# Kernel tuning notes

Measured on AMD Instinct MI355X. Metric: run time of the kernel, lower is better.

The kernel has to match this reference:

```python
import jax, jax.numpy as jnp
import numpy as np

S1 = (42, 1600, 1408); S2 = (21, 800, 704); S3 = (11, 400, 352); S4 = (6, 200, 176)
OFF = np.array([[dz, dy, dx] for dz in (-1, 0, 1) for dy in (-1, 0, 1) for dx in (-1, 0, 1)], np.int64)
KOFF = np.array([[kz, ky, kx] for kz in (0, 1, 2) for ky in (0, 1, 2) for kx in (0, 1, 2)], np.int64)

def _keys(c, s):
    return (c[:, 0] * s[1] + c[:, 1]) * s[2] + c[:, 2]

def _lookup(skeys, qk, valid):
    pos = np.searchsorted(skeys, qk)
    posc = np.clip(pos, 0, len(skeys) - 1)
    found = valid & (skeys[posc] == qk)
    return np.where(found, posc, -1).astype(np.int32)

def _subm_nbr(coords, skeys, shape):
    N = len(coords); nbr = np.empty((N, 27), np.int32); sh = np.array(shape)
    for t in range(27):
        q = coords + OFF[t]
        valid = np.all((q >= 0) & (q < sh), axis=1)
        nbr[:, t] = _lookup(skeys, _keys(q, shape), valid)
    return nbr

def _inv_nbr(fcoords, ckeys, cshape):
    # inverse of stride-2, pad-1, k-3 sparse conv: coarse = (fine + 1 - k) / 2
    N = len(fcoords); nbr = np.empty((N, 27), np.int32); csh = np.array(cshape)
    for t in range(27):
        cand = fcoords + 1 - KOFF[t]
        valid = np.all(cand >= 0, axis=1) & np.all(cand % 2 == 0, axis=1)
        cc = cand // 2
        valid &= np.all(cc < csh, axis=1)
        nbr[:, t] = _lookup(ckeys, _keys(cc, cshape), valid)
    return nbr

def _geometry():
    rng = np.random.default_rng(0)
    n = 130000
    c = np.stack([rng.integers(0, S1[i], n) for i in range(3)], 1).astype(np.int64)
    uk, idx = np.unique(_keys(c, S1), return_index=True)
    c1 = c[idx][:100000]; k1 = uk[:len(c1)]
    def down(cf, s):
        cc = cf // 2
        uk, idx = np.unique(_keys(cc, s), return_index=True)
        return cc[idx], uk
    c2, k2 = down(c1, S2); c3, k3 = down(c2, S3); c4, k4 = down(c3, S4)
    return dict(nbr4=_subm_nbr(c4, k4, S4), inv43=_inv_nbr(c3, k4, S4),
                nbr3=_subm_nbr(c3, k3, S3), inv32=_inv_nbr(c2, k3, S3),
                nbr2=_subm_nbr(c2, k2, S2), inv21=_inv_nbr(c1, k2, S2),
                nbr1=_subm_nbr(c1, k1, S1), n4=len(c4), n1=len(c1))

_SPECS = [("m4", 64, 64), ("i4", 64, 64), ("m3", 64, 64), ("i3", 64, 32),
          ("m2", 32, 32), ("i2", 32, 16), ("m1", 16, 16), ("c5", 16, 3)]

def _params(key):
    p = {}
    for i, (nm, ci, co) in enumerate(_SPECS):
        k = jax.random.fold_in(key, i)
        p["W_" + nm] = jax.random.normal(k, (27, ci, co), jnp.float32) * (1.0 / np.sqrt(27.0 * ci))
        p["g_" + nm] = jnp.ones((co,), jnp.float32)
        p["b_" + nm] = jnp.zeros((co,), jnp.float32)
    return p

def setup_inputs() -> dict:
    geo = _geometry()
    key = jax.random.key(0)
    inp = {k: jnp.asarray(v) for k, v in geo.items() if k.startswith(("nbr", "inv"))}
    inp["x"] = jax.random.normal(jax.random.fold_in(key, 100), (geo["n4"], 64), jnp.float32)
    inp.update(_params(key))
    return inp

def _block(f, nbr, W, g, b, relu=True):
    # gather-GEMM (sparse conv), then BatchNorm1d (training mode, eps=1e-3), then ReLU
    m = nbr >= 0                                             # [N,27]
    x = jnp.where(m[..., None], f[jnp.maximum(nbr, 0)], 0.0)  # [N,27,Cin]
    y = jnp.einsum('nkc,kcd->nd', x, W)                      # [N,Cout]
    mu = y.mean(0); var = y.var(0)
    y = (y - mu) * jax.lax.rsqrt(var + 1e-3) * g + b
    return jax.nn.relu(y) if relu else y

def reference(x, nbr4, inv43, nbr3, inv32, nbr2, inv21, nbr1,
              W_m4, g_m4, b_m4, W_i4, g_i4, b_i4, W_m3, g_m3, b_m3, W_i3, g_i3, b_i3,
              W_m2, g_m2, b_m2, W_i2, g_i2, b_i2, W_m1, g_m1, b_m1, W_c5, g_c5, b_c5):
    h = _block(x, nbr4, W_m4, g_m4, b_m4)      # subm4: [N4,64]
    h = _block(h, inv43, W_i4, g_i4, b_i4)     # inverse conv4 -> [N3,64]
    h = _block(h, nbr3, W_m3, g_m3, b_m3)      # subm3
    h = _block(h, inv32, W_i3, g_i3, b_i3)     # inverse conv3 -> [N2,32]
    h = _block(h, nbr2, W_m2, g_m2, b_m2)      # subm2
    h = _block(h, inv21, W_i2, g_i2, b_i2)     # inverse conv2 -> [N1,16]
    h = _block(h, nbr1, W_m1, g_m1, b_m1)      # subm1
    return _block(h, nbr1, W_c5, g_c5, b_c5, relu=False)  # conv5 (shares subm1 rulebook), BN only
```

## Files before the change

### kernel.cpp

```cpp
#include <hip/hip_runtime.h>

typedef _Float16 HALF;
typedef _Float16 f16x8 __attribute__((ext_vector_type(8)));
typedef float f32x4 __attribute__((ext_vector_type(4)));
typedef int i32x4 __attribute__((ext_vector_type(4)));

struct WArgs { const float* W[8]; HALF* dst[8]; };

__global__ void convert_all_w_kernel(WArgs a)
{
    const int CIs[8]  = {64, 64, 64, 64, 32, 32, 16, 16};
    const int COs[8]  = {64, 64, 64, 32, 32, 16, 16, 3};
    const int COPs[8] = {64, 64, 64, 32, 32, 16, 16, 16};
    const int L = blockIdx.y;
    const int CI = CIs[L], CO = COs[L], COP = COPs[L];
    const int K = 27 * CI, KP = (K + 31) & ~31;
    const int total = COP * KP;
    for (int i = blockIdx.x * 256 + threadIdx.x; i < total; i += gridDim.x * 256) {
        int jp = i / KP;
        int kp = i - jp * KP;
        float v = (jp < CO && kp < K) ? a.W[L][(size_t)kp * CO + jp] : 0.f;
        a.dst[L][((size_t)(kp >> 5) * COP + jp) * 32 + (kp & 31)] = (HALF)v;
    }
}

__global__ void convert_x_kernel(const float* __restrict__ x, HALF* __restrict__ xh, int total)
{
    int i = blockIdx.x * 256 + threadIdx.x;
    if (i < total) xh[i] = (HALF)x[i];
}

template<int CI, int CO_PAD, int NMT, bool FUSED>
__global__ __launch_bounds__(256, 2) void conv_kernel(
    const HALF* __restrict__ h, const int* __restrict__ nbr,
    const HALF* __restrict__ Wt, HALF* __restrict__ yout,
    float* __restrict__ sums, int n,
    const float* __restrict__ psums, const float* __restrict__ pg,
    const float* __restrict__ pb, float pinvn)
{
    constexpr int K    = 27 * CI;
    constexpr int KP   = (K + 31) & ~31;
    constexpr int NCH  = KP / 32;
    constexpr int NJB  = CO_PAD / 16;
    constexpr int NW   = 4;
    constexpr int NCB  = (CI >= 64) ? 2 : 1;
    constexpr int LOG2CI = (CI == 64) ? 6 : ((CI == 32) ? 5 : 4);
    constexpr int NIDX = (CI == 16) ? 14 : 27;

    __shared__ float red[2][NW][CO_PAD];

    const int wv   = threadIdx.x >> 6;
    const int lane = threadIdx.x & 63;
    const int l15  = lane & 15;
    const int lq   = lane >> 4;
    const int waveRow = blockIdx.x * (NW * 16 * NMT) + wv * (16 * NMT);

    f32x4 acc[NMT][NJB];
#pragma unroll
    for (int mt = 0; mt < NMT; ++mt)
#pragma unroll
        for (int jb = 0; jb < NJB; ++jb)
#pragma unroll
            for (int r = 0; r < 4; ++r) acc[mt][jb][r] = 0.f;

    int idxr[NMT][NIDX];
#pragma unroll
    for (int mt = 0; mt < NMT; ++mt) {
        const int row  = waveRow + mt * 16 + l15;
        const bool rok = row < n;
        const int* nb  = nbr + (size_t)min(row, n - 1) * 27;
#pragma unroll
        for (int s = 0; s < NIDX; ++s) {
            const int t = (CI == 16) ? (2 * s + (lq >> 1)) : s;
            const int v = nb[t < 27 ? t : 26];
            idxr[mt][s] = (rok && t < 27) ? v : -1;
        }
    }

    f16x8 sc8[NCB], bi8[NCB];
    if constexpr (FUSED) {
#pragma unroll
        for (int cb = 0; cb < NCB; ++cb) {
            const int c0 = cb * 32 + ((lq * 8) & (CI - 1));
#pragma unroll
            for (int j = 0; j < 8; ++j) {
                const int c = c0 + j;
                const float mu  = psums[c] * pinvn;
                const float var = psums[CI + c] * pinvn - mu * mu;
                const float sc  = rsqrtf(var + 1e-3f) * pg[c];
                sc8[cb][j] = (HALF)sc;
                bi8[cb][j] = (HALF)(pb[c] - mu * sc);
            }
        }
    }

#pragma unroll
    for (int kc = 0; kc < NCH; ++kc) {
        const int c   = (kc * 32 + lq * 8) & (CI - 1);
        const int slot = (CI == 64) ? (kc >> 1) : kc;
        const int ccb  = (NCB == 2) ? (kc & 1) : 0;

        const HALF* wb = Wt + (size_t)kc * (CO_PAD * 32) + lq * 8;
        f16x8 b[NJB];
#pragma unroll
        for (int jb = 0; jb < NJB; ++jb)
            b[jb] = *(const f16x8*)(wb + (size_t)(jb * 16 + l15) * 32);

#pragma unroll
        for (int mt = 0; mt < NMT; ++mt) {
            const int idx = idxr[mt][slot];
            const int off = (max(idx, 0) << LOG2CI) + c;
            f16x8 a = *(const f16x8*)(h + off);
            if constexpr (FUSED) {
                a = a * sc8[ccb] + bi8[ccb];
#pragma unroll
                for (int j = 0; j < 8; ++j)
                    a[j] = (a[j] < (HALF)0.f) ? (HALF)0.f : a[j];
            }
            const int m = ~(idx >> 31);
            i32x4 ai = __builtin_bit_cast(i32x4, a);
            ai.x &= m; ai.y &= m; ai.z &= m; ai.w &= m;
            a = __builtin_bit_cast(f16x8, ai);
#pragma unroll
            for (int jb = 0; jb < NJB; ++jb)
                acc[mt][jb] = __builtin_amdgcn_mfma_f32_16x16x32_f16(a, b[jb], acc[mt][jb], 0, 0, 0);
        }
    }

#pragma unroll
    for (int jb = 0; jb < NJB; ++jb) {
        const int col = jb * 16 + l15;
        float s = 0.f, sq = 0.f;
#pragma unroll
        for (int mt = 0; mt < NMT; ++mt) {
            const int rb = waveRow + mt * 16 + lq * 4;
#pragma unroll
            for (int r = 0; r < 4; ++r) {
                if (rb + r < n) {
                    const float v = acc[mt][jb][r];
                    yout[(size_t)(rb + r) * CO_PAD + col] = (HALF)v;
                    s += v;
                    sq += v * v;
                }
            }
        }
        s  += __shfl_xor(s, 16);  s  += __shfl_xor(s, 32);
        sq += __shfl_xor(sq, 16); sq += __shfl_xor(sq, 32);
        if (lane < 16) { red[0][wv][col] = s; red[1][wv][col] = sq; }
    }
    __syncthreads();
    if (threadIdx.x < CO_PAD) {
        float s = 0.f, sq = 0.f;
#pragma unroll
        for (int w = 0; w < NW; ++w) { s += red[0][w][threadIdx.x]; sq += red[1][w][threadIdx.x]; }
        atomicAdd(&sums[threadIdx.x], s);
        atomicAdd(&sums[CO_PAD + threadIdx.x], sq);
    }
}

__global__ void bn_out_kernel(const HALF* __restrict__ y, const float* __restrict__ sums,
                              const float* __restrict__ g, const float* __restrict__ b,
                              int n, float invn, float* __restrict__ out)
{
    int i = blockIdx.x * 256 + threadIdx.x;
    if (i >= n * 3) return;
    int row = i / 3;
    int c = i - row * 3;
    float mu  = sums[c] * invn;
    float var = sums[16 + c] * invn - mu * mu;
    float sc  = rsqrtf(var + 1e-3f) * g[c];
    out[i] = ((float)y[(size_t)row * 16 + c] - mu) * sc + b[c];
}

extern "C" void kernel_launch(void* const* d_in, const int* in_sizes, int n_in,
                              void* d_out, int out_size, void* d_ws, size_t ws_size,
                              hipStream_t stream)
{
    const int* nbr4  = (const int*)d_in[0];
    const int* inv43 = (const int*)d_in[1];
    const int* nbr3  = (const int*)d_in[2];
    const int* inv32 = (const int*)d_in[3];
    const int* nbr2  = (const int*)d_in[4];
    const int* inv21 = (const int*)d_in[5];
    const int* nbr1  = (const int*)d_in[6];
    const float* x   = (const float*)d_in[7];

    const int n4 = in_sizes[0] / 27;
    const int n3 = in_sizes[1] / 27;
    const int n2 = in_sizes[3] / 27;
    const int n1 = in_sizes[5] / 27;

    const int CIs[8]  = {64, 64, 64, 64, 32, 32, 16, 16};
    const int COPs[8] = {64, 64, 64, 32, 32, 16, 16, 16};
    int KPs[8], wtoff[8];
    int wtot = 0;
    for (int s = 0; s < 8; ++s) {
        KPs[s] = ((27 * CIs[s] + 31) / 32) * 32;
        wtoff[s] = wtot;
        wtot += COPs[s] * KPs[s];
    }

    char* ws = (char*)d_ws;
    HALF* wt = (HALF*)ws;
    size_t off = ((size_t)wtot * sizeof(HALF) + 255) & ~(size_t)255;
    float* sums = (float*)(ws + off);
    off += 8 * 128 * sizeof(float);
    off = (off + 255) & ~(size_t)255;
    HALF* xh = (HALF*)(ws + off);
    off += ((size_t)n4 * 64 * sizeof(HALF) + 255) & ~(size_t)255;
    size_t bufElems = 0;
    {
        size_t cand[4] = {(size_t)n4 * 64, (size_t)n3 * 64, (size_t)n2 * 32, (size_t)n1 * 16};
        for (int i = 0; i < 4; ++i) if (cand[i] > bufElems) bufElems = cand[i];
    }
    HALF* Y0 = (HALF*)(ws + off);
    off += (bufElems * sizeof(HALF) + 255) & ~(size_t)255;
    HALF* Y1 = (HALF*)(ws + off);

    hipMemsetAsync(sums, 0, 8 * 128 * sizeof(float), stream);

    WArgs wa;
    for (int s = 0; s < 8; ++s) { wa.W[s] = (const float*)d_in[8 + 3 * s]; wa.dst[s] = wt + wtoff[s]; }
    {
        int maxTotal = 64 * KPs[0];
        dim3 grid((maxTotal + 255) / 256, 8);
        convert_all_w_kernel<<<grid, 256, 0, stream>>>(wa);
    }
    convert_x_kernel<<<(n4 * 64 + 255) / 256, 256, 0, stream>>>(x, xh, n4 * 64);

#define G(s) ((const float*)d_in[9 + 3 * (s)])
#define B(s) ((const float*)d_in[10 + 3 * (s)])
#define SUMS(s) (sums + (s) * 128)
#define GRID(nn) (((nn) + 127) / 128)

    conv_kernel<64, 64, 2, false><<<GRID(n4), 256, 0, stream>>>(
        xh, nbr4, wt + wtoff[0], Y0, SUMS(0), n4, nullptr, nullptr, nullptr, 0.f);
    conv_kernel<64, 64, 2, true><<<GRID(n3), 256, 0, stream>>>(
        Y0, inv43, wt + wtoff[1], Y1, SUMS(1), n3, SUMS(0), G(0), B(0), 1.f / n4);
    conv_kernel<64, 64, 2, true><<<GRID(n3), 256, 0, stream>>>(
        Y1, nbr3, wt + wtoff[2], Y0, SUMS(2), n3, SUMS(1), G(1), B(1), 1.f / n3);
    conv_kernel<64, 32, 2, true><<<GRID(n2), 256, 0, stream>>>(
        Y0, inv32, wt + wtoff[3], Y1, SUMS(3), n2, SUMS(2), G(2), B(2), 1.f / n3);
    conv_kernel<32, 32, 2, true><<<GRID(n2), 256, 0, stream>>>(
        Y1, nbr2, wt + wtoff[4], Y0, SUMS(4), n2, SUMS(3), G(3), B(3), 1.f / n2);
    conv_kernel<32, 16, 2, true><<<GRID(n1), 256, 0, stream>>>(
        Y0, inv21, wt + wtoff[5], Y1, SUMS(5), n1, SUMS(4), G(4), B(4), 1.f / n2);
    conv_kernel<16, 16, 2, true><<<GRID(n1), 256, 0, stream>>>(
        Y1, nbr1, wt + wtoff[6], Y0, SUMS(6), n1, SUMS(5), G(5), B(5), 1.f / n1);
    conv_kernel<16, 16, 2, true><<<GRID(n1), 256, 0, stream>>>(
        Y0, nbr1, wt + wtoff[7], Y1, SUMS(7), n1, SUMS(6), G(6), B(6), 1.f / n1);
    bn_out_kernel<<<(n1 * 3 + 255) / 256, 256, 0, stream>>>(
        Y1, SUMS(7), G(7), B(7), n1, 1.f / n1, (float*)d_out);

#undef G
#undef B
#undef SUMS
#undef GRID
}
```

Before: 571.6 us.

## Software-pipeline neighbor gathers two chunks ahead and remap blocks across XCDs

Stops preloading all 27 neighbor indices into registers at kernel start. Indices and gathered feature vectors are now fetched two K-chunks ahead in a double-buffered register pipeline, so gather latency overlaps the MFMA work. Block IDs are also remapped so that consecutive row tiles land on the same XCD, which should improve L2 locality. The change lowers register use from the index array but adds dependent index-then-feature loads inside the loop. For CI=64 the same index is loaded twice.

```diff
diff --git a/kernel.cpp b/kernel.cpp
--- a/kernel.cpp
+++ b/kernel.cpp
@@ -45,7 +45,6 @@
     constexpr int NW   = 4;
     constexpr int NCB  = (CI >= 64) ? 2 : 1;
     constexpr int LOG2CI = (CI == 64) ? 6 : ((CI == 32) ? 5 : 4);
-    constexpr int NIDX = (CI == 16) ? 14 : 27;
 
     __shared__ float red[2][NW][CO_PAD];
 
@@ -53,7 +52,15 @@
     const int lane = threadIdx.x & 63;
     const int l15  = lane & 15;
     const int lq   = lane >> 4;
-    const int waveRow = blockIdx.x * (NW * 16 * NMT) + wv * (16 * NMT);
+
+    int bid = blockIdx.x;
+    {
+        const int nwg = gridDim.x;
+        const int q = nwg >> 3, r = nwg & 7;
+        const int xcd = bid & 7, idx = bid >> 3;
+        bid = (xcd < r ? xcd * (q + 1) : r * (q + 1) + (xcd - r) * q) + idx;
+    }
+    const int waveRow = bid * (NW * 16 * NMT) + wv * (16 * NMT);
 
     f32x4 acc[NMT][NJB];
 #pragma unroll
@@ -63,18 +70,13 @@
 #pragma unroll
             for (int r = 0; r < 4; ++r) acc[mt][jb][r] = 0.f;
 
-    int idxr[NMT][NIDX];
+    int  nbo[NMT];
+    bool rok[NMT];
 #pragma unroll
     for (int mt = 0; mt < NMT; ++mt) {
-        const int row  = waveRow + mt * 16 + l15;
-        const bool rok = row < n;
-        const int* nb  = nbr + (size_t)min(row, n - 1) * 27;
-#pragma unroll
-        for (int s = 0; s < NIDX; ++s) {
-            const int t = (CI == 16) ? (2 * s + (lq >> 1)) : s;
-            const int v = nb[t < 27 ? t : 26];
-            idxr[mt][s] = (rok && t < 27) ? v : -1;
-        }
+        const int row = waveRow + mt * 16 + l15;
+        rok[mt] = row < n;
+        nbo[mt] = min(row, n - 1) * 27;
     }
 
     f16x8 sc8[NCB], bi8[NCB];
@@ -94,11 +96,27 @@
         }
     }
 
+    #define TAPOF(kc) ((CI == 16) ? (2 * (kc) + (lq >> 1)) : ((CI == 64) ? ((kc) >> 1) : (kc)))
+    #define CHOF(kc)  (((kc) * 32 + lq * 8) & (CI - 1))
+
+    int   ipf[2][NMT];
+    f16x8 apf[2][NMT];
+#pragma unroll
+    for (int p = 0; p < 2; ++p) {
+#pragma unroll
+        for (int mt = 0; mt < NMT; ++mt) {
+            const int t   = TAPOF(p);
+            const int v   = nbr[nbo[mt] + (t < 27 ? t : 26)];
+            const int idx = (rok[mt] && t < 27) ? v : -1;
+            ipf[p][mt] = idx;
+            apf[p][mt] = *(const f16x8*)(h + ((max(idx, 0) << LOG2CI) + CHOF(p)));
+        }
+    }
+
 #pragma unroll
     for (int kc = 0; kc < NCH; ++kc) {
-        const int c   = (kc * 32 + lq * 8) & (CI - 1);
-        const int slot = (CI == 64) ? (kc >> 1) : kc;
-        const int ccb  = (NCB == 2) ? (kc & 1) : 0;
+        const int cur = kc & 1;
+        const int ccb = (NCB == 2) ? (kc & 1) : 0;
 
         const HALF* wb = Wt + (size_t)kc * (CO_PAD * 32) + lq * 8;
         f16x8 b[NJB];
@@ -106,18 +124,32 @@
         for (int jb = 0; jb < NJB; ++jb)
             b[jb] = *(const f16x8*)(wb + (size_t)(jb * 16 + l15) * 32);
 
+        f16x8 a_use[NMT];
+        int   i_use[NMT];
+#pragma unroll
+        for (int mt = 0; mt < NMT; ++mt) { a_use[mt] = apf[cur][mt]; i_use[mt] = ipf[cur][mt]; }
+
+        if (kc + 2 < NCH) {
+#pragma unroll
+            for (int mt = 0; mt < NMT; ++mt) {
+                const int t   = TAPOF(kc + 2);
+                const int v   = nbr[nbo[mt] + (t < 27 ? t : 26)];
+                const int idx = (rok[mt] && t < 27) ? v : -1;
+                ipf[cur][mt] = idx;
+                apf[cur][mt] = *(const f16x8*)(h + ((max(idx, 0) << LOG2CI) + CHOF(kc + 2)));
+            }
+        }
+
 #pragma unroll
         for (int mt = 0; mt < NMT; ++mt) {
-            const int idx = idxr[mt][slot];
-            const int off = (max(idx, 0) << LOG2CI) + c;
-            f16x8 a = *(const f16x8*)(h + off);
+            f16x8 a = a_use[mt];
             if constexpr (FUSED) {
                 a = a * sc8[ccb] + bi8[ccb];
 #pragma unroll
                 for (int j = 0; j < 8; ++j)
                     a[j] = (a[j] < (HALF)0.f) ? (HALF)0.f : a[j];
             }
-            const int m = ~(idx >> 31);
+            const int m = ~(i_use[mt] >> 31);
             i32x4 ai = __builtin_bit_cast(i32x4, a);
             ai.x &= m; ai.y &= m; ai.z &= m; ai.w &= m;
             a = __builtin_bit_cast(f16x8, ai);
@@ -126,6 +158,8 @@
                 acc[mt][jb] = __builtin_amdgcn_mfma_f32_16x16x32_f16(a, b[jb], acc[mt][jb], 0, 0, 0);
         }
     }
+    #undef TAPOF
+    #undef CHOF
 
 #pragma unroll
     for (int jb = 0; jb < NJB; ++jb) {
```

New measurement: 568.1 us. Within noise of the previous version (-0.6%).

## Software-pipeline gather loads with inline asm, stage rulebook in LDS, remap blocks per XCD

Applied to the files above, without the earlier changes.

Neighbor indices for the block are now staged in shared memory instead of being held in per-thread registers. The A-gather and weight loads are issued through inline-asm global loads three chunks ahead, with explicit vmcnt waits, so memory latency overlaps the MFMA work. Block IDs are also remapped so consecutive rows land on the same XCD, which should improve L2 locality. The cost is fragile manual waitcnt accounting, extra LDS traffic and a syncthreads per block, and more live registers for the prefetch slots.

```diff
diff --git a/kernel.cpp b/kernel.cpp
--- a/kernel.cpp
+++ b/kernel.cpp
@@ -30,6 +30,17 @@
     if (i < total) xh[i] = (HALF)x[i];
 }
 
+#define WAITV(N) do { \
+    if      ((N) == 18) asm volatile("s_waitcnt vmcnt(18)" ::: "memory"); \
+    else if ((N) == 12) asm volatile("s_waitcnt vmcnt(12)" ::: "memory"); \
+    else if ((N) == 9)  asm volatile("s_waitcnt vmcnt(9)"  ::: "memory"); \
+    else if ((N) == 8)  asm volatile("s_waitcnt vmcnt(8)"  ::: "memory"); \
+    else if ((N) == 6)  asm volatile("s_waitcnt vmcnt(6)"  ::: "memory"); \
+    else if ((N) == 4)  asm volatile("s_waitcnt vmcnt(4)"  ::: "memory"); \
+    else if ((N) == 3)  asm volatile("s_waitcnt vmcnt(3)"  ::: "memory"); \
+    else                asm volatile("s_waitcnt vmcnt(0)"  ::: "memory"); \
+} while (0)
+
 template<int CI, int CO_PAD, int NMT, bool FUSED>
 __global__ __launch_bounds__(256, 2) void conv_kernel(
     const HALF* __restrict__ h, const int* __restrict__ nbr,
@@ -45,36 +56,32 @@
     constexpr int NW   = 4;
     constexpr int NCB  = (CI >= 64) ? 2 : 1;
     constexpr int LOG2CI = (CI == 64) ? 6 : ((CI == 32) ? 5 : 4);
-    constexpr int NIDX = (CI == 16) ? 14 : 27;
-
+    constexpr int ROWS = NW * 16 * NMT;
+    constexpr int PD   = 3;
+    constexpr int EV   = NMT + NJB;
+
+    __shared__ int   lidx[ROWS * 27];
     __shared__ float red[2][NW][CO_PAD];
 
     const int wv   = threadIdx.x >> 6;
     const int lane = threadIdx.x & 63;
     const int l15  = lane & 15;
     const int lq   = lane >> 4;
-    const int waveRow = blockIdx.x * (NW * 16 * NMT) + wv * (16 * NMT);
-
-    f32x4 acc[NMT][NJB];
-#pragma unroll
-    for (int mt = 0; mt < NMT; ++mt)
-#pragma unroll
-        for (int jb = 0; jb < NJB; ++jb)
-#pragma unroll
-            for (int r = 0; r < 4; ++r) acc[mt][jb][r] = 0.f;
-
-    int idxr[NMT][NIDX];
-#pragma unroll
-    for (int mt = 0; mt < NMT; ++mt) {
-        const int row  = waveRow + mt * 16 + l15;
-        const bool rok = row < n;
-        const int* nb  = nbr + (size_t)min(row, n - 1) * 27;
-#pragma unroll
-        for (int s = 0; s < NIDX; ++s) {
-            const int t = (CI == 16) ? (2 * s + (lq >> 1)) : s;
-            const int v = nb[t < 27 ? t : 26];
-            idxr[mt][s] = (rok && t < 27) ? v : -1;
-        }
+
+    int bid = blockIdx.x;
+    {
+        const int nwg = gridDim.x;
+        const int q = nwg >> 3, r = nwg & 7;
+        const int xcd = bid & 7, idx = bid >> 3;
+        bid = (xcd < r ? xcd * (q + 1) : r * (q + 1) + (xcd - r) * q) + idx;
+    }
+    const int blockRow0 = bid * ROWS;
+    const int waveRow   = blockRow0 + wv * (16 * NMT);
+
+    for (int i = threadIdx.x; i < ROWS * 27; i += 256) {
+        const int r   = i / 27;
+        const int row = blockRow0 + r;
+        lidx[i] = (row < n) ? nbr[(size_t)row * 27 + (i - r * 27)] : -1;
     }
 
     f16x8 sc8[NCB], bi8[NCB];
@@ -94,38 +101,112 @@
         }
     }
 
+    f32x4 acc[NMT][NJB];
+#pragma unroll
+    for (int mt = 0; mt < NMT; ++mt)
+#pragma unroll
+        for (int jb = 0; jb < NJB; ++jb)
+#pragma unroll
+            for (int r = 0; r < 4; ++r) acc[mt][jb][r] = 0.f;
+
+    int lb[NMT];
+#pragma unroll
+    for (int mt = 0; mt < NMT; ++mt) lb[mt] = (wv * (16 * NMT) + mt * 16 + l15) * 27;
+
+    __syncthreads();
+    asm volatile("s_waitcnt vmcnt(0)" ::: "memory");
+    __builtin_amdgcn_sched_barrier(0);
+
+    #define TAPOF(kc_) ((CI == 16) ? (2 * (kc_) + (lq >> 1)) : ((CI == 64) ? ((kc_) >> 1) : (kc_)))
+    #define CHOF(kc_)  ((((kc_) * 32) + lq * 8) & (CI - 1))
+    #define GIDX(s_, mt_) ({ const int t_ = TAPOF(s_); (t_ < 27) ? lidx[lb[mt_] + t_] : -1; })
+
+    i32x4 ar[PD][NMT];
+    i32x4 br[PD][NJB];
+    int   ip[PD][NMT];
+
+    #define ISSUE_A(s_, slot_, mt_, idxv_) do { \
+        const int iv_ = (idxv_); \
+        ip[slot_][mt_] = iv_; \
+        const HALF* pa_ = h + (((iv_ < 0 ? 0 : iv_) << LOG2CI) + CHOF(s_)); \
+        asm volatile("global_load_dwordx4 %0, %1, off" : "=v"(ar[slot_][mt_]) : "v"(pa_)); \
+    } while (0)
+
+    #define ISSUE_B(s_, slot_) do { \
+        const HALF* pb_ = Wt + (size_t)(s_) * (CO_PAD * 32) + l15 * 32 + lq * 8; \
+        asm volatile("global_load_dwordx4 %0, %1, off" : "=v"(br[slot_][0]) : "v"(pb_)); \
+        if constexpr (NJB > 1) asm volatile("global_load_dwordx4 %0, %1, off offset:1024" : "=v"(br[slot_][1]) : "v"(pb_)); \
+        if constexpr (NJB > 2) asm volatile("global_load_dwordx4 %0, %1, off offset:2048" : "=v"(br[slot_][2]) : "v"(pb_)); \
+        if constexpr (NJB > 3) asm volatile("global_load_dwordx4 %0, %1, off offset:3072" : "=v"(br[slot_][3]) : "v"(pb_)); \
+    } while (0)
+
+#pragma unroll
+    for (int s = 0; s < PD; ++s) {
+#pragma unroll
+        for (int mt = 0; mt < NMT; ++mt) { const int iv = GIDX(s, mt); ISSUE_A(s, s, mt, iv); }
+        ISSUE_B(s, s);
+    }
+    int idn[NMT];
+#pragma unroll
+    for (int mt = 0; mt < NMT; ++mt) idn[mt] = GIDX(PD, mt);
+
 #pragma unroll
     for (int kc = 0; kc < NCH; ++kc) {
-        const int c   = (kc * 32 + lq * 8) & (CI - 1);
-        const int slot = (CI == 64) ? (kc >> 1) : kc;
+        const int slot = kc % PD;
         const int ccb  = (NCB == 2) ? (kc & 1) : 0;
 
-        const HALF* wb = Wt + (size_t)kc * (CO_PAD * 32) + lq * 8;
-        f16x8 b[NJB];
-#pragma unroll
-        for (int jb = 0; jb < NJB; ++jb)
-            b[jb] = *(const f16x8*)(wb + (size_t)(jb * 16 + l15) * 32);
+        i32x4 av[NMT]; int im[NMT];
+#pragma unroll
+        for (int mt = 0; mt < NMT; ++mt) { av[mt] = ar[slot][mt]; im[mt] = ip[slot][mt]; }
+        i32x4 bv[NJB];
+#pragma unroll
+        for (int jb = 0; jb < NJB; ++jb) bv[jb] = br[slot][jb];
+
+        if (kc + PD < NCH) {
+#pragma unroll
+            for (int mt = 0; mt < NMT; ++mt) ISSUE_A(kc + PD, slot, mt, idn[mt]);
+            ISSUE_B(kc + PD, slot);
+        }
+        if (kc + PD + 1 < NCH) {
+#pragma unroll
+            for (int mt = 0; mt < NMT; ++mt) idn[mt] = GIDX(kc + PD + 1, mt);
+        }
+
+        {
+            const int hi = (kc < NCH - 1 - PD) ? kc : (NCH - 1 - PD);
+            int nq = hi - (kc - PD);
+            if (nq < 0) nq = 0;
+            if (nq > PD) nq = PD;
+            const int w = EV * nq;
+            WAITV(w);
+        }
+        __builtin_amdgcn_sched_barrier(0);
 
 #pragma unroll
         for (int mt = 0; mt < NMT; ++mt) {
-            const int idx = idxr[mt][slot];
-            const int off = (max(idx, 0) << LOG2CI) + c;
-            f16x8 a = *(const f16x8*)(h + off);
+            f16x8 a = __builtin_bit_cast(f16x8, av[mt]);
             if constexpr (FUSED) {
                 a = a * sc8[ccb] + bi8[ccb];
 #pragma unroll
                 for (int j = 0; j < 8; ++j)
                     a[j] = (a[j] < (HALF)0.f) ? (HALF)0.f : a[j];
             }
-            const int m = ~(idx >> 31);
+            const int m = ~(im[mt] >> 31);
             i32x4 ai = __builtin_bit_cast(i32x4, a);
             ai.x &= m; ai.y &= m; ai.z &= m; ai.w &= m;
             a = __builtin_bit_cast(f16x8, ai);
 #pragma unroll
             for (int jb = 0; jb < NJB; ++jb)
-                acc[mt][jb] = __builtin_amdgcn_mfma_f32_16x16x32_f16(a, b[jb], acc[mt][jb], 0, 0, 0);
-        }
-    }
+                acc[mt][jb] = __builtin_amdgcn_mfma_f32_16x16x32_f16(
+                    a, __builtin_bit_cast(f16x8, bv[jb]), acc[mt][jb], 0, 0, 0);
+        }
+    }
+
+    #undef TAPOF
+    #undef CHOF
+    #undef GIDX
+    #undef ISSUE_A
+    #undef ISSUE_B
 
 #pragma unroll
     for (int jb = 0; jb < NJB; ++jb) {
```

Result: slower. 722.2 us (+26.4%).
